# Kernel optimization log

Measured on AMD Instinct MI355X. Metric: run time of the kernel, lower is better.

## Reference

```python
import jax, jax.numpy as jnp
import numpy as np

C = 19          # EEG channels
NP = C * C      # 361 channel pairs
D = 256         # UNIFIED_FEATURE_DIM
H = 8           # num_heads
HD = D // H     # head dim


def _build_mask():
    # rel[p, q] = True iff key-pair q shares a channel with query-pair p
    idx = np.arange(NP)
    ci, cj = idx // C, idx % C
    rel = ((ci[:, None] == ci[None, :]) | (ci[:, None] == cj[None, :]) |
           (cj[:, None] == ci[None, :]) | (cj[:, None] == cj[None, :]))
    return jnp.asarray(rel.reshape(C, C, NP))  # (channel_i, j, key_pair)

MASK = _build_mask()


def setup_inputs() -> dict:
    key = jax.random.key(0)
    ks = jax.random.split(key, 6)
    s = 0.05
    return {
        "x": jax.random.normal(ks[0], (32, NP, D), jnp.float32),
        # 19 stacked nn.MultiheadAttention modules: in_proj (3D, D) = [Wq; Wk; Wv]
        "w_in": jax.random.normal(ks[1], (C, 3 * D, D), jnp.float32) * s,
        "b_in": jnp.zeros((C, 3 * D), jnp.float32),
        "w_out": jax.random.normal(ks[2], (C, D, D), jnp.float32) * s,
        "b_out": jnp.zeros((C, D), jnp.float32),
        # fusion: nn.Linear(D, D)
        "w_fuse": jax.random.normal(ks[3], (D, D), jnp.float32) * s,
        "b_fuse": jnp.zeros((D,), jnp.float32),
    }


def reference(x, w_in, b_in, w_out, b_out, w_fuse, b_fuse):
    # x: (B, 361, D). Pair p=(i,j) at index i*19+j uses attention module i,
    # query = x[:, p], keys/values = pairs sharing channel i or j (mask).
    B = x.shape[0]
    wq, wk, wv = w_in[:, :D], w_in[:, D:2 * D], w_in[:, 2 * D:]
    bq, bk, bv = b_in[:, :D], b_in[:, D:2 * D], b_in[:, 2 * D:]

    # Per-channel K/V projections over all 361 pairs: (C, B, NP, D)
    K = jnp.einsum('bnd,ced->cbne', x, wk) + bk[:, None, None, :]
    V = jnp.einsum('bnd,ced->cbne', x, wv) + bv[:, None, None, :]
    # Queries grouped by first channel i: x reshaped to (B, C, C, D)
    xq = x.reshape(B, C, C, D)
    Q = jnp.einsum('bcjd,ced->cbje', xq, wq) + bq[:, None, None, :]  # (C,B,C,D)

    Qh = Q.reshape(C, B, C, H, HD)
    Kh = K.reshape(C, B, NP, H, HD)
    Vh = V.reshape(C, B, NP, H, HD)

    scale = 1.0 / jnp.sqrt(jnp.asarray(HD, x.dtype))
    scores = jnp.einsum('cbqhe,cbkhe->cbhqk', Qh, Kh) * scale  # (C,B,H,C,NP)
    scores = jnp.where(MASK[:, None, None, :, :], scores, -jnp.inf)
    attn = jax.nn.softmax(scores, axis=-1)

    out = jnp.einsum('cbhqk,cbkhe->cbqhe', attn, Vh).reshape(C, B, C, D)
    out = jnp.einsum('cbqd,ced->cbqe', out, w_out) + b_out[:, None, None, :]
    out = out.transpose(1, 0, 2, 3).reshape(B, NP, D)  # back to (B, 361, D)

    # fusion ('linear') + residual
    return out @ w_fuse.T + b_fuse + x
```

## Files before the change

kernel.cpp:

```cpp
#include <hip/hip_runtime.h>

#define CC 19
#define NPOS 361
#define NPAD 384
#define DIM 256
#define TKEY 32
#define NTILES 12

#define LDS_BYTES 128000

using bf16x8 = __attribute__((ext_vector_type(8))) short;
using f16x4  = __attribute__((ext_vector_type(4))) _Float16;
using floatx4 = __attribute__((ext_vector_type(4))) float;
using uintx2 = __attribute__((ext_vector_type(2))) unsigned int;

__device__ __forceinline__ unsigned short f2bf(float f) {
  unsigned u = __builtin_bit_cast(unsigned, f);
  u += 0x7fffu + ((u >> 16) & 1u);
  return (unsigned short)(u >> 16);
}

__device__ __forceinline__ unsigned short f2h(float f) {
  auto h = __builtin_amdgcn_cvt_pkrtz(f, 0.f);
  return (unsigned short)(__builtin_bit_cast(unsigned, h) & 0xffffu);
}

__global__ void conv_all_kernel(const float* __restrict__ x,
                                const float* __restrict__ w_in,
                                const float* __restrict__ w_out,
                                const float* __restrict__ w_fuse,
                                unsigned short* __restrict__ ws) {
  const int j = blockIdx.x * 256 + threadIdx.x;
  float4 v = make_float4(0.f, 0.f, 0.f, 0.f);
  unsigned short* dst;
  if (j < 786432) {
    const int row = j >> 6;
    const int off = (j & 63) << 2;
    const int b = row / NPAD;
    const int r = row - b * NPAD;
    if (r < NPOS) v = *(const float4*)&x[(b * NPOS + r) * DIM + off];
    dst = &ws[row * DIM + off];
  } else if (j < 1720320) {
    const int k = j - 786432;
    v = *(const float4*)&w_in[k << 2];
    dst = &ws[3145728 + (k << 2)];
  } else if (j < 2031616) {
    const int k = j - 1720320;
    v = *(const float4*)&w_out[k << 2];
    dst = &ws[6881280 + (k << 2)];
  } else {
    const int k = j - 2031616;
    v = *(const float4*)&w_fuse[k << 2];
    dst = &ws[8126464 + (k << 2)];
  }
  ushort4 o;
  o.x = f2bf(v.x); o.y = f2bf(v.y); o.z = f2bf(v.z); o.w = f2bf(v.w);
  *(ushort4*)dst = o;
}

__launch_bounds__(512, 2)
__global__ void cgca_kernel(const float* __restrict__ xf,
                            const float* __restrict__ b_in,
                            const float* __restrict__ b_out,
                            const float* __restrict__ b_fuse,
                            const unsigned short* __restrict__ xbf,
                            const unsigned short* __restrict__ wibf,
                            const unsigned short* __restrict__ wobf,
                            const unsigned short* __restrict__ wfbf,
                            float* __restrict__ out) {
  const int bid = blockIdx.x;
  const int xcd = bid & 7;
  const int slot = bid >> 3;
  int c, b;
  if (slot < 64) {
    c = ((slot >> 5) << 3) + xcd;
    b = slot & 31;
  } else {
    const int widx = ((slot - 64) << 3) + xcd;
    c = 16 + (widx >> 5);
    b = widx & 31;
  }

  const int tid = threadIdx.x;
  const int w = tid >> 6;
  const int lane = tid & 63;
  const int quad = lane >> 4;
  const int l16 = lane & 15;

  extern __shared__ char smem[];
  unsigned short* sQ    = (unsigned short*)(smem);
  unsigned short* bufx0 = (unsigned short*)(smem + 16896);
  unsigned short* bufx1 = (unsigned short*)(smem + 16896 + 16896);
  unsigned short* sK0   = (unsigned short*)(smem + 50688);
  unsigned short* sK1   = (unsigned short*)(smem + 50688 + 16896);
  unsigned short* sVT0  = (unsigned short*)(smem + 84480);
  unsigned short* sVT1  = (unsigned short*)(smem + 84480 + 21760);

  const float scale = 0.17677669529663687f;
  const floatx4 fzero = {0.f, 0.f, 0.f, 0.f};

  for (int i = tid; i < 2 * 16 * 40; i += 512) {
    const int buf = i >= 640;
    const int idx = buf ? (i - 640) : i;
    const int row = idx / 40;
    const int col = idx - row * 40;
    unsigned short val = (row == 0) ? (unsigned short)0x3C00 : (unsigned short)0;
    (buf ? sVT1 : sVT0)[(256 + row) * 40 + col] = val;
  }

  {
    const int eh0 = w * 32;
#pragma unroll
    for (int mt = 0; mt < 2; ++mt) {
      const int xrow = b * NPAD + c * CC + mt * 16 + l16;
      bf16x8 a8[8];
#pragma unroll
      for (int k = 0; k < 8; ++k)
        a8[k] = *(const bf16x8*)&xbf[xrow * DIM + k * 32 + quad * 8];
#pragma unroll
      for (int nt2 = 0; nt2 < 2; ++nt2) {
        const int e0 = eh0 + nt2 * 16;
        floatx4 acc = fzero;
#pragma unroll
        for (int k = 0; k < 8; ++k) {
          bf16x8 b8 = *(const bf16x8*)&wibf[(c * 768 + e0 + l16) * DIM + k * 32 + quad * 8];
          acc = __builtin_amdgcn_mfma_f32_16x16x32_bf16(a8[k], b8, acc, 0, 0, 0);
        }
        const float bias = b_in[c * 768 + e0 + l16];
#pragma unroll
        for (int r = 0; r < 4; ++r)
          sQ[(mt * 16 + quad * 4 + r) * 264 + e0 + l16] = f2bf((acc[r] + bias) * scale);
      }
    }
  }

  const int wrow0 = c * 768 + 256 + w * 64;
  bf16x8 wreg[4][8];
#pragma unroll
  for (int m4 = 0; m4 < 4; ++m4)
#pragma unroll
    for (int k = 0; k < 8; ++k)
      wreg[m4][k] = *(const bf16x8*)&wibf[(wrow0 + m4 * 16 + l16) * DIM + k * 32 + quad * 8];

  float ba[4][4];
#pragma unroll
  for (int m4 = 0; m4 < 4; ++m4) {
    const float4 bv = *(const float4*)&b_in[wrow0 + m4 * 16 + quad * 4];
    ba[m4][0] = bv.x; ba[m4][1] = bv.y; ba[m4][2] = bv.z; ba[m4][3] = bv.w;
  }

#pragma unroll
  for (int it = 0; it < 2; ++it) {
    const int cc2 = tid + it * 512;
    const int row = cc2 >> 5;
    const int col = (cc2 & 31) * 8;
    *(bf16x8*)&bufx0[row * 264 + col] = *(const bf16x8*)&xbf[(b * NPAD + row) * DIM + col];
  }

  floatx4 o_acc[2][2];
  floatx4 lacc[2];
#pragma unroll
  for (int mt = 0; mt < 2; ++mt) {
#pragma unroll
    for (int nt2 = 0; nt2 < 2; ++nt2) o_acc[mt][nt2] = fzero;
    lacc[mt] = fzero;
  }
  const int eh = w * 32;

  __syncthreads();

  bf16x8 aqr[2];
#pragma unroll
  for (int mt = 0; mt < 2; ++mt)
    aqr[mt] = *(const bf16x8*)&sQ[(mt * 16 + l16) * 264 + eh + quad * 8];

  for (int t = 0; t < NTILES; ++t) {
    const int t0 = t * TKEY;
    unsigned short* bx  = (t & 1) ? bufx1 : bufx0;
    unsigned short* bxn = (t & 1) ? bufx0 : bufx1;
    unsigned short* sK  = (t & 1) ? sK1 : sK0;
    unsigned short* sVT = (t & 1) ? sVT1 : sVT0;

    if (t + 1 < NTILES) {
#pragma unroll
      for (int it = 0; it < 2; ++it) {
        const int cc2 = tid + it * 512;
        const int row = cc2 >> 5;
        const int col = (cc2 & 31) * 8;
        *(bf16x8*)&bxn[row * 264 + col] =
            *(const bf16x8*)&xbf[(b * NPAD + t0 + TKEY + row) * DIM + col];
      }
    }

    {
      floatx4 acc[4][2];
#pragma unroll
      for (int m4 = 0; m4 < 4; ++m4)
#pragma unroll
        for (int n4 = 0; n4 < 2; ++n4) acc[m4][n4] = fzero;

#pragma unroll
      for (int k = 0; k < 8; ++k) {
        bf16x8 bfr[2];
#pragma unroll
        for (int n4 = 0; n4 < 2; ++n4)
          bfr[n4] = *(const bf16x8*)&bx[(n4 * 16 + l16) * 264 + k * 32 + quad * 8];
#pragma unroll
        for (int m4 = 0; m4 < 4; ++m4)
#pragma unroll
          for (int n4 = 0; n4 < 2; ++n4)
            acc[m4][n4] = __builtin_amdgcn_mfma_f32_16x16x32_bf16(wreg[m4][k], bfr[n4],
                                                                  acc[m4][n4], 0, 0, 0);
      }
#pragma unroll
      for (int m4 = 0; m4 < 4; ++m4) {
#pragma unroll
        for (int n4 = 0; n4 < 2; ++n4) {
          const int key = n4 * 16 + l16;
          if (w < 4) {
            const int e0 = w * 64 + m4 * 16 + quad * 4;
            ushort4 pk;
            pk.x = f2bf(acc[m4][n4][0] + ba[m4][0]);
            pk.y = f2bf(acc[m4][n4][1] + ba[m4][1]);
            pk.z = f2bf(acc[m4][n4][2] + ba[m4][2]);
            pk.w = f2bf(acc[m4][n4][3] + ba[m4][3]);
            *(ushort4*)&sK[key * 264 + e0] = pk;
          } else {
            const int e0 = (w - 4) * 64 + m4 * 16 + quad * 4;
#pragma unroll
            for (int r = 0; r < 4; ++r)
              sVT[(e0 + r) * 40 + key] = f2h(acc[m4][n4][r] + ba[m4][r]);
          }
        }
      }
    }
    __syncthreads();

#pragma unroll
    for (int mt = 0; mt < 2; ++mt) {
      f16x4 ap[2];
#pragma unroll
      for (int n4 = 0; n4 < 2; ++n4) {
        const bf16x8 bk = *(const bf16x8*)&sK[(n4 * 16 + l16) * 264 + eh + quad * 8];
        const floatx4 scT = __builtin_amdgcn_mfma_f32_16x16x32_bf16(bk, aqr[mt], fzero, 0, 0, 0);
        const int kbase = t0 + n4 * 16 + quad * 4;
        const unsigned q = (unsigned)(mt * 16 + l16);
        float p[4];
#pragma unroll
        for (int r = 0; r < 4; ++r) {
          const int kabs = kbase + r;
          const unsigned ki = ((unsigned)kabs * 110377u) >> 21;
          const unsigned kj = (unsigned)kabs - ki * 19u;
          const bool ok = (kabs < NPOS) &&
                          (ki == (unsigned)c || kj == (unsigned)c || ki == q || kj == q);
          p[r] = ok ? __expf(scT[r]) : 0.f;
        }
        const auto h01 = __builtin_amdgcn_cvt_pkrtz(p[0], p[1]);
        const auto h23 = __builtin_amdgcn_cvt_pkrtz(p[2], p[3]);
        uintx2 uv = {__builtin_bit_cast(unsigned, h01), __builtin_bit_cast(unsigned, h23)};
        ap[n4] = __builtin_bit_cast(f16x4, uv);
      }
#pragma unroll
      for (int n4 = 0; n4 < 2; ++n4) {
#pragma unroll
        for (int nt2 = 0; nt2 < 2; ++nt2) {
          const f16x4 bv =
              *(const f16x4*)&sVT[(eh + nt2 * 16 + l16) * 40 + n4 * 16 + quad * 4];
          o_acc[mt][nt2] =
              __builtin_amdgcn_mfma_f32_16x16x16f16(ap[n4], bv, o_acc[mt][nt2], 0, 0, 0);
        }
        const f16x4 bo = *(const f16x4*)&sVT[(256 + l16) * 40 + n4 * 16 + quad * 4];
        lacc[mt] = __builtin_amdgcn_mfma_f32_16x16x16f16(ap[n4], bo, lacc[mt], 0, 0, 0);
      }
    }
  }

#pragma unroll
  for (int mt = 0; mt < 2; ++mt) {
    float invl[4];
#pragma unroll
    for (int r = 0; r < 4; ++r) {
      const float l = __shfl(lacc[mt][r], (lane & 48));
      invl[r] = 1.f / l;
    }
#pragma unroll
    for (int nt2 = 0; nt2 < 2; ++nt2)
#pragma unroll
      for (int r = 0; r < 4; ++r)
        bufx0[(mt * 16 + quad * 4 + r) * 264 + eh + nt2 * 16 + l16] =
            f2bf(o_acc[mt][nt2][r] * invl[r]);
  }
  __syncthreads();

#pragma unroll
  for (int mt = 0; mt < 2; ++mt) {
    bf16x8 a8[8];
#pragma unroll
    for (int k = 0; k < 8; ++k)
      a8[k] = *(const bf16x8*)&bufx0[(mt * 16 + l16) * 264 + k * 32 + quad * 8];
#pragma unroll
    for (int nt2 = 0; nt2 < 2; ++nt2) {
      const int e0 = w * 32 + nt2 * 16;
      floatx4 acc = fzero;
#pragma unroll
      for (int k = 0; k < 8; ++k) {
        bf16x8 b8 = *(const bf16x8*)&wobf[(c * 256 + e0 + l16) * DIM + k * 32 + quad * 8];
        acc = __builtin_amdgcn_mfma_f32_16x16x32_bf16(a8[k], b8, acc, 0, 0, 0);
      }
      const float bias = b_out[c * 256 + e0 + l16];
#pragma unroll
      for (int r = 0; r < 4; ++r)
        sK0[(mt * 16 + quad * 4 + r) * 264 + e0 + l16] = f2bf(acc[r] + bias);
    }
  }
  __syncthreads();

#pragma unroll
  for (int mt = 0; mt < 2; ++mt) {
    bf16x8 a8[8];
#pragma unroll
    for (int k = 0; k < 8; ++k)
      a8[k] = *(const bf16x8*)&sK0[(mt * 16 + l16) * 264 + k * 32 + quad * 8];
#pragma unroll
    for (int nt2 = 0; nt2 < 2; ++nt2) {
      const int e0 = w * 32 + nt2 * 16;
      floatx4 acc = fzero;
#pragma unroll
      for (int k = 0; k < 8; ++k) {
        bf16x8 b8 = *(const bf16x8*)&wfbf[(e0 + l16) * DIM + k * 32 + quad * 8];
        acc = __builtin_amdgcn_mfma_f32_16x16x32_bf16(a8[k], b8, acc, 0, 0, 0);
      }
      const float bfu = b_fuse[e0 + l16];
#pragma unroll
      for (int r = 0; r < 4; ++r) {
        const int row = mt * 16 + quad * 4 + r;
        if (row < CC) {
          const int gp = (b * NPOS + c * CC + row) * DIM + e0 + l16;
          out[gp] = acc[r] + bfu + xf[gp];
        }
      }
    }
  }
}

extern "C" void kernel_launch(void* const* d_in, const int* in_sizes, int n_in,
                              void* d_out, int out_size, void* d_ws, size_t ws_size,
                              hipStream_t stream) {
  const float* x      = (const float*)d_in[0];
  const float* w_in   = (const float*)d_in[1];
  const float* b_in   = (const float*)d_in[2];
  const float* w_out  = (const float*)d_in[3];
  const float* b_out  = (const float*)d_in[4];
  const float* w_fuse = (const float*)d_in[5];
  const float* b_fuse = (const float*)d_in[6];
  float* out = (float*)d_out;

  if (ws_size < (size_t)16384000) return;

  unsigned short* ws = (unsigned short*)d_ws;
  unsigned short* x_bf  = ws;
  unsigned short* wi_bf = ws + 3145728;
  unsigned short* wo_bf = ws + 6881280;
  unsigned short* wf_bf = ws + 8126464;

  conv_all_kernel<<<8000, 256, 0, stream>>>(x, w_in, w_out, w_fuse, ws);

  (void)hipFuncSetAttribute((const void*)cgca_kernel,
                            hipFuncAttributeMaxDynamicSharedMemorySize, LDS_BYTES);
  cgca_kernel<<<608, 512, LDS_BYTES, stream>>>(x, b_in, b_out, b_fuse, x_bf, wi_bf,
                                               wo_bf, wf_bf, out);
}
```

Measured before the change: 285.1 us.

## Keep per-head K/V/Q projections in registers instead of staging through LDS

Result: faster. 253.6 us (-11.0%).

```diff
diff --git a/kernel.cpp b/kernel.cpp
--- a/kernel.cpp
+++ b/kernel.cpp
@@ -7,7 +7,7 @@
 #define TKEY 32
 #define NTILES 12
 
-#define LDS_BYTES 128000
+#define LDS_BYTES 33792
 
 using bf16x8 = __attribute__((ext_vector_type(8))) short;
 using f16x4  = __attribute__((ext_vector_type(4))) _Float16;
@@ -20,9 +20,11 @@
   return (unsigned short)(u >> 16);
 }
 
-__device__ __forceinline__ unsigned short f2h(float f) {
-  auto h = __builtin_amdgcn_cvt_pkrtz(f, 0.f);
-  return (unsigned short)(__builtin_bit_cast(unsigned, h) & 0xffffu);
+__device__ __forceinline__ f16x4 pack4h(float a, float b, float c2, float d) {
+  const auto h01 = __builtin_amdgcn_cvt_pkrtz(a, b);
+  const auto h23 = __builtin_amdgcn_cvt_pkrtz(c2, d);
+  uintx2 uv = {__builtin_bit_cast(unsigned, h01), __builtin_bit_cast(unsigned, h23)};
+  return __builtin_bit_cast(f16x4, uv);
 }
 
 __global__ void conv_all_kernel(const float* __restrict__ x,
@@ -86,68 +88,68 @@
   const int lane = tid & 63;
   const int quad = lane >> 4;
   const int l16 = lane & 15;
+  const int eh = w * 32;
 
   extern __shared__ char smem[];
-  unsigned short* sQ    = (unsigned short*)(smem);
-  unsigned short* bufx0 = (unsigned short*)(smem + 16896);
-  unsigned short* bufx1 = (unsigned short*)(smem + 16896 + 16896);
-  unsigned short* sK0   = (unsigned short*)(smem + 50688);
-  unsigned short* sK1   = (unsigned short*)(smem + 50688 + 16896);
-  unsigned short* sVT0  = (unsigned short*)(smem + 84480);
-  unsigned short* sVT1  = (unsigned short*)(smem + 84480 + 21760);
+  unsigned short* bufx0 = (unsigned short*)(smem);
+  unsigned short* bufx1 = (unsigned short*)(smem + 16896);
+  float* sL = (float*)(smem + 16896);
 
   const float scale = 0.17677669529663687f;
   const floatx4 fzero = {0.f, 0.f, 0.f, 0.f};
 
-  for (int i = tid; i < 2 * 16 * 40; i += 512) {
-    const int buf = i >= 640;
-    const int idx = buf ? (i - 640) : i;
-    const int row = idx / 40;
-    const int col = idx - row * 40;
-    unsigned short val = (row == 0) ? (unsigned short)0x3C00 : (unsigned short)0;
-    (buf ? sVT1 : sVT0)[(256 + row) * 40 + col] = val;
-  }
-
+  f16x4 qf[2][2];
   {
-    const int eh0 = w * 32;
+    bf16x8 wq[2][8];
+#pragma unroll
+    for (int m4 = 0; m4 < 2; ++m4)
+#pragma unroll
+      for (int k = 0; k < 8; ++k)
+        wq[m4][k] = *(const bf16x8*)&wibf[(c * 768 + eh + m4 * 16 + l16) * DIM + k * 32 + quad * 8];
+    float bq[2][4];
+#pragma unroll
+    for (int m4 = 0; m4 < 2; ++m4) {
+      const float4 bv4 = *(const float4*)&b_in[c * 768 + eh + m4 * 16 + quad * 4];
+      bq[m4][0] = bv4.x; bq[m4][1] = bv4.y; bq[m4][2] = bv4.z; bq[m4][3] = bv4.w;
+    }
 #pragma unroll
     for (int mt = 0; mt < 2; ++mt) {
       const int xrow = b * NPAD + c * CC + mt * 16 + l16;
-      bf16x8 a8[8];
+      bf16x8 xq[8];
 #pragma unroll
       for (int k = 0; k < 8; ++k)
-        a8[k] = *(const bf16x8*)&xbf[xrow * DIM + k * 32 + quad * 8];
-#pragma unroll
-      for (int nt2 = 0; nt2 < 2; ++nt2) {
-        const int e0 = eh0 + nt2 * 16;
+        xq[k] = *(const bf16x8*)&xbf[xrow * DIM + k * 32 + quad * 8];
+#pragma unroll
+      for (int m4 = 0; m4 < 2; ++m4) {
         floatx4 acc = fzero;
 #pragma unroll
-        for (int k = 0; k < 8; ++k) {
-          bf16x8 b8 = *(const bf16x8*)&wibf[(c * 768 + e0 + l16) * DIM + k * 32 + quad * 8];
-          acc = __builtin_amdgcn_mfma_f32_16x16x32_bf16(a8[k], b8, acc, 0, 0, 0);
-        }
-        const float bias = b_in[c * 768 + e0 + l16];
-#pragma unroll
-        for (int r = 0; r < 4; ++r)
-          sQ[(mt * 16 + quad * 4 + r) * 264 + e0 + l16] = f2bf((acc[r] + bias) * scale);
-      }
-    }
-  }
-
-  const int wrow0 = c * 768 + 256 + w * 64;
-  bf16x8 wreg[4][8];
-#pragma unroll
-  for (int m4 = 0; m4 < 4; ++m4)
-#pragma unroll
-    for (int k = 0; k < 8; ++k)
-      wreg[m4][k] = *(const bf16x8*)&wibf[(wrow0 + m4 * 16 + l16) * DIM + k * 32 + quad * 8];
-
-  float ba[4][4];
-#pragma unroll
-  for (int m4 = 0; m4 < 4; ++m4) {
-    const float4 bv = *(const float4*)&b_in[wrow0 + m4 * 16 + quad * 4];
-    ba[m4][0] = bv.x; ba[m4][1] = bv.y; ba[m4][2] = bv.z; ba[m4][3] = bv.w;
-  }
+        for (int k = 0; k < 8; ++k)
+          acc = __builtin_amdgcn_mfma_f32_16x16x32_bf16(wq[m4][k], xq[k], acc, 0, 0, 0);
+        qf[mt][m4] = pack4h((acc[0] + bq[m4][0]) * scale, (acc[1] + bq[m4][1]) * scale,
+                            (acc[2] + bq[m4][2]) * scale, (acc[3] + bq[m4][3]) * scale);
+      }
+    }
+  }
+
+  bf16x8 wk[2][8], wv[2][8];
+#pragma unroll
+  for (int m4 = 0; m4 < 2; ++m4)
+#pragma unroll
+    for (int k = 0; k < 8; ++k) {
+      wk[m4][k] =
+          *(const bf16x8*)&wibf[(c * 768 + 256 + eh + m4 * 16 + l16) * DIM + k * 32 + quad * 8];
+      wv[m4][k] =
+          *(const bf16x8*)&wibf[(c * 768 + 512 + eh + m4 * 16 + l16) * DIM + k * 32 + quad * 8];
+    }
+  float bk[2][4];
+#pragma unroll
+  for (int m4 = 0; m4 < 2; ++m4) {
+    const float4 bv4 = *(const float4*)&b_in[c * 768 + 256 + eh + m4 * 16 + quad * 4];
+    bk[m4][0] = bv4.x; bk[m4][1] = bv4.y; bk[m4][2] = bv4.z; bk[m4][3] = bv4.w;
+  }
+  float bV[2];
+#pragma unroll
+  for (int ne = 0; ne < 2; ++ne) bV[ne] = b_in[c * 768 + 512 + eh + ne * 16 + l16];
 
 #pragma unroll
   for (int it = 0; it < 2; ++it) {
@@ -158,28 +160,18 @@
   }
 
   floatx4 o_acc[2][2];
-  floatx4 lacc[2];
-#pragma unroll
-  for (int mt = 0; mt < 2; ++mt) {
-#pragma unroll
-    for (int nt2 = 0; nt2 < 2; ++nt2) o_acc[mt][nt2] = fzero;
-    lacc[mt] = fzero;
-  }
-  const int eh = w * 32;
+  float lsum[2] = {0.f, 0.f};
+#pragma unroll
+  for (int mt = 0; mt < 2; ++mt)
+#pragma unroll
+    for (int ne = 0; ne < 2; ++ne) o_acc[mt][ne] = fzero;
 
   __syncthreads();
-
-  bf16x8 aqr[2];
-#pragma unroll
-  for (int mt = 0; mt < 2; ++mt)
-    aqr[mt] = *(const bf16x8*)&sQ[(mt * 16 + l16) * 264 + eh + quad * 8];
 
   for (int t = 0; t < NTILES; ++t) {
     const int t0 = t * TKEY;
     unsigned short* bx  = (t & 1) ? bufx1 : bufx0;
     unsigned short* bxn = (t & 1) ? bufx0 : bufx1;
-    unsigned short* sK  = (t & 1) ? sK1 : sK0;
-    unsigned short* sVT = (t & 1) ? sVT1 : sVT0;
 
     if (t + 1 < NTILES) {
 #pragma unroll
@@ -192,59 +184,48 @@
       }
     }
 
-    {
-      floatx4 acc[4][2];
-#pragma unroll
-      for (int m4 = 0; m4 < 4; ++m4)
-#pragma unroll
-        for (int n4 = 0; n4 < 2; ++n4) acc[m4][n4] = fzero;
-
-#pragma unroll
-      for (int k = 0; k < 8; ++k) {
-        bf16x8 bfr[2];
-#pragma unroll
-        for (int n4 = 0; n4 < 2; ++n4)
-          bfr[n4] = *(const bf16x8*)&bx[(n4 * 16 + l16) * 264 + k * 32 + quad * 8];
-#pragma unroll
-        for (int m4 = 0; m4 < 4; ++m4)
-#pragma unroll
-          for (int n4 = 0; n4 < 2; ++n4)
-            acc[m4][n4] = __builtin_amdgcn_mfma_f32_16x16x32_bf16(wreg[m4][k], bfr[n4],
-                                                                  acc[m4][n4], 0, 0, 0);
-      }
-#pragma unroll
-      for (int m4 = 0; m4 < 4; ++m4) {
+    floatx4 aK[2][2], aV[2][2];
+#pragma unroll
+    for (int i = 0; i < 2; ++i)
+#pragma unroll
+      for (int j = 0; j < 2; ++j) { aK[i][j] = fzero; aV[i][j] = fzero; }
+#pragma unroll
+    for (int k = 0; k < 8; ++k) {
+      bf16x8 xfr[2];
+#pragma unroll
+      for (int n4 = 0; n4 < 2; ++n4)
+        xfr[n4] = *(const bf16x8*)&bx[(n4 * 16 + l16) * 264 + k * 32 + quad * 8];
+#pragma unroll
+      for (int m4 = 0; m4 < 2; ++m4)
 #pragma unroll
         for (int n4 = 0; n4 < 2; ++n4) {
-          const int key = n4 * 16 + l16;
-          if (w < 4) {
-            const int e0 = w * 64 + m4 * 16 + quad * 4;
-            ushort4 pk;
-            pk.x = f2bf(acc[m4][n4][0] + ba[m4][0]);
-            pk.y = f2bf(acc[m4][n4][1] + ba[m4][1]);
-            pk.z = f2bf(acc[m4][n4][2] + ba[m4][2]);
-            pk.w = f2bf(acc[m4][n4][3] + ba[m4][3]);
-            *(ushort4*)&sK[key * 264 + e0] = pk;
-          } else {
-            const int e0 = (w - 4) * 64 + m4 * 16 + quad * 4;
-#pragma unroll
-            for (int r = 0; r < 4; ++r)
-              sVT[(e0 + r) * 40 + key] = f2h(acc[m4][n4][r] + ba[m4][r]);
-          }
+          aK[m4][n4] = __builtin_amdgcn_mfma_f32_16x16x32_bf16(wk[m4][k], xfr[n4], aK[m4][n4], 0, 0, 0);
+          aV[n4][m4] = __builtin_amdgcn_mfma_f32_16x16x32_bf16(xfr[n4], wv[m4][k], aV[n4][m4], 0, 0, 0);
         }
-      }
     }
     __syncthreads();
 
+    f16x4 kf[2][2];
+    f16x4 vf[2][2];
+#pragma unroll
+    for (int kt = 0; kt < 2; ++kt)
+#pragma unroll
+      for (int ec = 0; ec < 2; ++ec) {
+        kf[kt][ec] = pack4h(aK[ec][kt][0] + bk[ec][0], aK[ec][kt][1] + bk[ec][1],
+                            aK[ec][kt][2] + bk[ec][2], aK[ec][kt][3] + bk[ec][3]);
+        vf[kt][ec] = pack4h(aV[kt][ec][0] + bV[ec], aV[kt][ec][1] + bV[ec],
+                            aV[kt][ec][2] + bV[ec], aV[kt][ec][3] + bV[ec]);
+      }
+
 #pragma unroll
     for (int mt = 0; mt < 2; ++mt) {
-      f16x4 ap[2];
-#pragma unroll
-      for (int n4 = 0; n4 < 2; ++n4) {
-        const bf16x8 bk = *(const bf16x8*)&sK[(n4 * 16 + l16) * 264 + eh + quad * 8];
-        const floatx4 scT = __builtin_amdgcn_mfma_f32_16x16x32_bf16(bk, aqr[mt], fzero, 0, 0, 0);
-        const int kbase = t0 + n4 * 16 + quad * 4;
-        const unsigned q = (unsigned)(mt * 16 + l16);
+      const unsigned q = (unsigned)(mt * 16 + l16);
+      f16x4 pf[2];
+#pragma unroll
+      for (int kt = 0; kt < 2; ++kt) {
+        floatx4 s = __builtin_amdgcn_mfma_f32_16x16x16f16(kf[kt][0], qf[mt][0], fzero, 0, 0, 0);
+        s = __builtin_amdgcn_mfma_f32_16x16x16f16(kf[kt][1], qf[mt][1], s, 0, 0, 0);
+        const int kbase = t0 + kt * 16 + quad * 4;
         float p[4];
 #pragma unroll
         for (int r = 0; r < 4; ++r) {
@@ -253,43 +234,44 @@
           const unsigned kj = (unsigned)kabs - ki * 19u;
           const bool ok = (kabs < NPOS) &&
                           (ki == (unsigned)c || kj == (unsigned)c || ki == q || kj == q);
-          p[r] = ok ? __expf(scT[r]) : 0.f;
+          p[r] = ok ? __expf(s[r]) : 0.f;
         }
-        const auto h01 = __builtin_amdgcn_cvt_pkrtz(p[0], p[1]);
-        const auto h23 = __builtin_amdgcn_cvt_pkrtz(p[2], p[3]);
-        uintx2 uv = {__builtin_bit_cast(unsigned, h01), __builtin_bit_cast(unsigned, h23)};
-        ap[n4] = __builtin_bit_cast(f16x4, uv);
-      }
-#pragma unroll
-      for (int n4 = 0; n4 < 2; ++n4) {
-#pragma unroll
-        for (int nt2 = 0; nt2 < 2; ++nt2) {
-          const f16x4 bv =
-              *(const f16x4*)&sVT[(eh + nt2 * 16 + l16) * 40 + n4 * 16 + quad * 4];
-          o_acc[mt][nt2] =
-              __builtin_amdgcn_mfma_f32_16x16x16f16(ap[n4], bv, o_acc[mt][nt2], 0, 0, 0);
-        }
-        const f16x4 bo = *(const f16x4*)&sVT[(256 + l16) * 40 + n4 * 16 + quad * 4];
-        lacc[mt] = __builtin_amdgcn_mfma_f32_16x16x16f16(ap[n4], bo, lacc[mt], 0, 0, 0);
-      }
+        lsum[mt] += (p[0] + p[1]) + (p[2] + p[3]);
+        pf[kt] = pack4h(p[0], p[1], p[2], p[3]);
+      }
+#pragma unroll
+      for (int kt = 0; kt < 2; ++kt)
+#pragma unroll
+        for (int ne = 0; ne < 2; ++ne)
+          o_acc[mt][ne] =
+              __builtin_amdgcn_mfma_f32_16x16x16f16(pf[kt], vf[kt][ne], o_acc[mt][ne], 0, 0, 0);
     }
   }
 
 #pragma unroll
   for (int mt = 0; mt < 2; ++mt) {
-    float invl[4];
-#pragma unroll
-    for (int r = 0; r < 4; ++r) {
-      const float l = __shfl(lacc[mt][r], (lane & 48));
-      invl[r] = 1.f / l;
-    }
-#pragma unroll
-    for (int nt2 = 0; nt2 < 2; ++nt2)
+    lsum[mt] += __shfl_xor(lsum[mt], 16);
+    lsum[mt] += __shfl_xor(lsum[mt], 32);
+  }
+  if (lane < 16) {
+    sL[w * 32 + lane] = lsum[0];
+    sL[w * 32 + 16 + lane] = lsum[1];
+  }
+  float invl[2][4];
+#pragma unroll
+  for (int mt = 0; mt < 2; ++mt)
+#pragma unroll
+    for (int r = 0; r < 4; ++r)
+      invl[mt][r] = 1.f / sL[w * 32 + mt * 16 + quad * 4 + r];
+
+#pragma unroll
+  for (int mt = 0; mt < 2; ++mt)
+#pragma unroll
+    for (int ne = 0; ne < 2; ++ne)
 #pragma unroll
       for (int r = 0; r < 4; ++r)
-        bufx0[(mt * 16 + quad * 4 + r) * 264 + eh + nt2 * 16 + l16] =
-            f2bf(o_acc[mt][nt2][r] * invl[r]);
-  }
+        bufx0[(mt * 16 + quad * 4 + r) * 264 + eh + ne * 16 + l16] =
+            f2bf(o_acc[mt][ne][r] * invl[mt][r]);
   __syncthreads();
 
 #pragma unroll
@@ -310,7 +292,7 @@
       const float bias = b_out[c * 256 + e0 + l16];
 #pragma unroll
       for (int r = 0; r < 4; ++r)
-        sK0[(mt * 16 + quad * 4 + r) * 264 + e0 + l16] = f2bf(acc[r] + bias);
+        bufx1[(mt * 16 + quad * 4 + r) * 264 + e0 + l16] = f2bf(acc[r] + bias);
     }
   }
   __syncthreads();
@@ -320,7 +302,7 @@
     bf16x8 a8[8];
 #pragma unroll
     for (int k = 0; k < 8; ++k)
-      a8[k] = *(const bf16x8*)&sK0[(mt * 16 + l16) * 264 + k * 32 + quad * 8];
+      a8[k] = *(const bf16x8*)&bufx1[(mt * 16 + l16) * 264 + k * 32 + quad * 8];
 #pragma unroll
     for (int nt2 = 0; nt2 < 2; ++nt2) {
       const int e0 = w * 32 + nt2 * 16;
```
